# Kernel optimization log

Hardware: AMD Instinct MI355X
Metric: run time of the kernel (lower is better)

The kernel has to match this reference:

```python
import jax, jax.numpy as jnp
import numpy as np

B, S, A, D, m, M = 131072, 274, 30, 128, 6, 8
H1, Z = 256, 4
EPS_SINK, N_SINK = 0.05, 10
ETA0, ETA1 = 0.05, 0.15
ALPHA_MIN, ALPHA_MAX = 0.06, 0.3
W_R, W_S, W_C = 0.6, 0.25, 0.15
TECH_IDX = np.array([61, 91, 121, 151, 181, 211, 241, 271])


def setup_inputs() -> dict:
    key = jax.random.key(0)
    ks = jax.random.split(key, 24)
    rn = lambda k, shp, fan: (jax.random.normal(k, shp, jnp.float32) / np.sqrt(fan)).astype(jnp.float32)
    return {
        'state': jax.random.normal(ks[0], (B, S), jnp.float32),
        'fitness': jnp.ones((B, M), jnp.float32),
        # epitope_encoder: Linear(S,256) -> LayerNorm -> ReLU -> Linear(256, m*D)
        'we1': rn(ks[1], (S, H1), S), 'be1': jnp.zeros((H1,)),
        'ln_g': jnp.ones((H1,)), 'ln_b': jnp.zeros((H1,)),
        'we2': rn(ks[2], (H1, m * D), H1), 'be2': jnp.zeros((m * D,)),
        'proto_keys': rn(ks[3], (M, D), D),
        # M decoder MLPs: Linear(D,128)->ReLU->Linear(128,A)->Softplus (stacked)
        'wd1': rn(ks[4], (M, D, 128), D), 'bd1': jnp.zeros((M, 128)),
        'wd2': rn(ks[5], (M, 128, A), 128), 'bd2': jnp.zeros((M, A)),
        # TCellMinimal: Linear(12,D)->ReLU; heads for crisis types z and crisis_base
        'wt': rn(ks[6], (12, D), 12), 'bt': jnp.zeros((D,)),
        'wz': rn(ks[7], (D, Z), D), 'bz': jnp.zeros((Z,)),
        'wc': rn(ks[8], (D, 1), D), 'bc': jnp.zeros((1,)),
        'w_prev': jnp.full((1, M), 1.0 / M, jnp.float32),
        'crisis_bias': jnp.zeros((1,), jnp.float32),
    }


def _forward(state, fitness, we1, be1, ln_g, ln_b, we2, be2, proto_keys,
             wd1, bd1, wd2, bd2, wt, bt, wz, bz, wc, bc, w_prev, crisis_bias):
    # ---- market feature extraction ----
    balance = state[:, 0:1]
    prices = state[:, 1:31]
    shares = state[:, 31:61]
    price_mean = prices.mean(axis=1, keepdims=True)
    price_std = jnp.std(prices, axis=1, keepdims=True, ddof=1) + 1e-8  # torch .std is unbiased
    total_value = balance + (prices * shares).sum(axis=1, keepdims=True)
    cash_ratio = balance / (total_value + 1e-8)
    tech = state[:, TECH_IDX]
    mf = jnp.concatenate([balance, price_mean, price_std, cash_ratio, tech], axis=1)  # [B,12]
    # ---- TCellMinimal (reconstructed) ----
    h_t = jax.nn.relu(mf @ wt + bt)                # danger embedding [B,D]
    z = jax.nn.softmax(h_t @ wz + bz, axis=-1)     # crisis types [B,Z]
    crisis_base = jax.nn.sigmoid(h_t @ wc + bc)    # [B,1]
    danger = h_t
    # ---- crisis level ----
    delta_sharpe = state[:, -2:-1]
    cvar = state[:, -1:]
    ds_s = jax.nn.sigmoid(delta_sharpe * 10.0)
    cv_s = jax.nn.sigmoid(jnp.abs(cvar) * 50.0)
    crisis_level = W_R * crisis_base + W_S * ds_s + W_C * cv_s + crisis_bias  # [B,1]
    # ---- epitope encoder (eval mode: dropout off) ----
    h = state @ we1 + be1
    mu = h.mean(axis=-1, keepdims=True)
    var = ((h - mu) ** 2).mean(axis=-1, keepdims=True)
    h = (h - mu) * jax.lax.rsqrt(var + 1e-5) * ln_g + ln_b
    h = jax.nn.relu(h)
    E = (h @ we2 + be2).reshape(B, m, D)
    # ---- IRT (reconstructed): cosine cost + Sinkhorn OT + replicator mix ----
    En = E / (jnp.linalg.norm(E, axis=-1, keepdims=True) + 1e-8)
    Kn = proto_keys / (jnp.linalg.norm(proto_keys, axis=-1, keepdims=True) + 1e-8)
    dn = danger / (jnp.linalg.norm(danger, axis=-1, keepdims=True) + 1e-8)
    sim = jnp.einsum('bmd,jd->bmj', En, Kn)          # [B,m,M]
    dsim = jnp.einsum('bd,jd->bj', dn, Kn)           # [B,M]
    C = 1.0 - sim - 0.1 * dsim[:, None, :]           # cost matrix [B,m,M]
    logK = -C / EPS_SINK
    log_mu = -jnp.log(float(m))
    log_nu = -jnp.log(float(M))
    u = jnp.zeros((B, m), C.dtype)
    v = jnp.zeros((B, M), C.dtype)
    for _ in range(N_SINK):
        u = log_mu - jax.nn.logsumexp(logK + v[:, None, :], axis=2)
        v = log_nu - jax.nn.logsumexp(logK + u[:, :, None], axis=1)
    P = jnp.exp(logK + u[:, :, None] + v[:, None, :])  # transport plan [B,m,M]
    w_ot = P.sum(axis=1)
    w_ot = w_ot / (w_ot.sum(axis=-1, keepdims=True) + 1e-8)
    eta = ETA0 + ETA1 * crisis_level                   # [B,1]
    w_rep = w_prev * jnp.exp(eta * fitness)
    w_rep = w_rep / (w_rep.sum(axis=-1, keepdims=True) + 1e-8)
    alpha_c = jnp.clip(ALPHA_MAX - (ALPHA_MAX - ALPHA_MIN) * crisis_level, ALPHA_MIN, ALPHA_MAX)
    w = (1.0 - alpha_c) * w_rep + alpha_c * w_ot
    w = w / (w.sum(axis=-1, keepdims=True) + 1e-8)     # [B,M]
    # ---- per-prototype decoders (note: input K[:,j,:] is batch-constant) ----
    hd = jax.nn.relu(jnp.einsum('jd,jdh->jh', proto_keys, wd1) + bd1)
    conc = jax.nn.softplus(jnp.einsum('jh,jha->ja', hd, wd2) + bd2)  # [M,A]
    mixed_conc = jnp.einsum('bm,ma->ba', w, conc) + 1.0
    # deterministic=True path (Dirichlet mean proxy via softmax as in source)
    action = jax.nn.softmax(mixed_conc, axis=-1)
    action = jnp.clip(action, 0.0, 1.0)
    action = action / (action.sum(axis=-1, keepdims=True) + 1e-8)
    return action


def reference(state, fitness, we1, be1, ln_g, ln_b, we2, be2, proto_keys,
              wd1, bd1, wd2, bd2, wt, bt, wz, bz, wc, bc, w_prev, crisis_bias):
    return _forward(state, fitness, we1, be1, ln_g, ln_b, we2, be2, proto_keys,
                    wd1, bd1, wd2, bd2, wt, bt, wz, bz, wc, bc, w_prev, crisis_bias)
```

## Files before the change

### kernel.cpp

```cpp
#include <hip/hip_runtime.h>
#include <math.h>

#define B_TOT   131072
#define S_DIM   274
#define H1_DIM  256
#define M_EMB   6
#define M_POP   8
#define D_DIM   128
#define A_DIM   30

typedef __attribute__((ext_vector_type(8))) short bf16x8;
typedef __attribute__((ext_vector_type(4))) float f32x4;

__device__ __forceinline__ float sigmf(float x){ return 1.0f/(1.0f+__expf(-x)); }

__device__ __forceinline__ unsigned short f2bf(float f){
    union { float f; unsigned int u; } v; v.f = f;
    unsigned int r = v.u + 0x7FFFu + ((v.u >> 16) & 1u);
    return (unsigned short)(r >> 16);
}

__device__ __forceinline__ bf16x8 pack8(const float* v){
    bf16x8 r;
    #pragma unroll
    for (int j=0;j<8;++j) r[j] = (short)f2bf(v[j]);
    return r;
}

__global__ void k0a_precompute(const float* __restrict__ proto,
                               const float* __restrict__ wd1, const float* __restrict__ bd1,
                               const float* __restrict__ wd2, const float* __restrict__ bd2,
                               const float* __restrict__ we2, const float* __restrict__ be2,
                               float* __restrict__ Kn, float* __restrict__ conc,
                               float* __restrict__ W2K, float* __restrict__ bK)
{
    __shared__ float sKn[M_POP][D_DIM];
    __shared__ float sHd[M_POP][D_DIM];
    const int t = threadIdx.x;
    const int j = t >> 5, lane32 = t & 31;
    float ss = 0.f;
    for (int q = lane32; q < D_DIM; q += 32){ float v = proto[j*D_DIM+q]; ss += v*v; }
    #pragma unroll
    for (int mk = 16; mk >= 1; mk >>= 1) ss += __shfl_xor(ss, mk, 64);
    float inv = 1.0f / (sqrtf(ss) + 1e-8f);
    for (int q = lane32; q < D_DIM; q += 32){
        float kv = proto[j*D_DIM+q]*inv;
        Kn[j*D_DIM+q] = kv; sKn[j][q] = kv;
    }
    for (int h = lane32; h < D_DIM; h += 32){
        float acc = bd1[j*D_DIM+h];
        for (int d = 0; d < D_DIM; ++d)
            acc = fmaf(proto[j*D_DIM+d], wd1[(j*D_DIM+d)*D_DIM + h], acc);
        sHd[j][h] = fmaxf(acc, 0.f);
    }
    __syncthreads();
    if (t < M_POP*A_DIM){
        int jj = t / A_DIM, a = t - jj*A_DIM;
        float acc = bd2[jj*A_DIM + a];
        for (int h = 0; h < D_DIM; ++h)
            acc = fmaf(sHd[jj][h], wd2[(jj*D_DIM+h)*A_DIM + a], acc);
        float sp;
        if (acc > 20.f)       sp = acc;
        else if (acc < -20.f) sp = expf(acc);
        else                  sp = log1pf(expf(acc));
        conc[jj*A_DIM + a] = sp;
    }
    for (int o = t; o < 256*48; o += 256){
        int k = o / 48, pc = o - k*48;
        int jj = pc & 7, col0 = (pc >> 3) * 128;
        const float4* wrow = (const float4*)(we2 + (size_t)k*768 + col0);
        const float4* krow = (const float4*)(&sKn[jj][0]);
        float4 s4 = make_float4(0.f,0.f,0.f,0.f);
        #pragma unroll 8
        for (int dq = 0; dq < 32; ++dq){
            float4 wv = wrow[dq], kv = krow[dq];
            s4.x = fmaf(wv.x,kv.x,s4.x); s4.y = fmaf(wv.y,kv.y,s4.y);
            s4.z = fmaf(wv.z,kv.z,s4.z); s4.w = fmaf(wv.w,kv.w,s4.w);
        }
        W2K[o] = (s4.x+s4.y)+(s4.z+s4.w);
    }
    if (t < 48){
        int jj = t & 7, col0 = (t >> 3) * 128;
        const float4* brow = (const float4*)(be2 + col0);
        const float4* krow = (const float4*)(&sKn[jj][0]);
        float4 s4 = make_float4(0.f,0.f,0.f,0.f);
        #pragma unroll 8
        for (int dq = 0; dq < 32; ++dq){
            float4 bv = brow[dq], kv = krow[dq];
            s4.x = fmaf(bv.x,kv.x,s4.x); s4.y = fmaf(bv.y,kv.y,s4.y);
            s4.z = fmaf(bv.z,kv.z,s4.z); s4.w = fmaf(bv.w,kv.w,s4.w);
        }
        bK[t] = (s4.x+s4.y)+(s4.z+s4.w);
    }
}

__global__ void k0b_we1_frag(const float* __restrict__ we1, short* __restrict__ B1f)
{
    int s = blockIdx.x*256 + threadIdx.x;
    int ct = s / (9*64);
    int rem = s - ct*(9*64);
    int ks = rem >> 6, lam = rem & 63;
    int kb = 32*ks + (lam>>4)*8;
    int col = 16*ct + (lam&15);
    float v[8];
    #pragma unroll
    for (int j=0;j<8;++j){
        int k = kb + j;
        v[j] = (k < S_DIM) ? we1[(size_t)k*H1_DIM + col] : 0.f;
    }
    bf16x8 p = pack8(v);
    *(bf16x8*)(B1f + (size_t)s*8) = p;
}

__global__ void k0c_we2_frag(const float* __restrict__ we2, const float* __restrict__ W2K,
                             short* __restrict__ B2f)
{
    int s = blockIdx.x*256 + threadIdx.x;
    int ct = s / (8*64);
    int rem = s - ct*(8*64);
    int ks = rem >> 6, lam = rem & 63;
    int kb = 32*ks + (lam>>4)*8;
    int col = 16*ct + (lam&15);
    float v[8];
    #pragma unroll
    for (int j=0;j<8;++j){
        int k = kb + j;
        v[j] = (col < 768) ? we2[(size_t)k*768 + col] : W2K[k*48 + (col-768)];
    }
    bf16x8 p = pack8(v);
    *(bf16x8*)(B2f + (size_t)s*8) = p;
}

__global__ __launch_bounds__(256, 2)
void k1_h1_aux(const float* __restrict__ state, const short* __restrict__ B1f,
               const float* __restrict__ be1, const float* __restrict__ lng,
               const float* __restrict__ lnb, const float* __restrict__ wt,
               const float* __restrict__ bt,  const float* __restrict__ wc,
               const float* __restrict__ bc,  const float* __restrict__ crisis_bias,
               const float* __restrict__ Kn,
               short* __restrict__ h1b, float* __restrict__ crisL, float* __restrict__ dsimO)
{
    __shared__ short ldsB[2][8192];
    const int tid  = threadIdx.x;
    const int lane = tid & 63, w = tid >> 6;
    const int grp  = lane >> 4;
    const int row0 = blockIdx.x * 128;

    {
        const int r = tid >> 1, part = tid & 1;
        const float* srow = state + (size_t)(row0 + r) * S_DIM;
        float bal = srow[0];
        float sp = 0.f;
        for (int q = 1; q <= 30; ++q) sp += srow[q];
        float pmean = sp * (1.0f/30.0f);
        float sv = 0.f, tv = bal;
        for (int q = 1; q <= 30; ++q){
            float p = srow[q];
            float d = p - pmean; sv = fmaf(d,d,sv);
            tv = fmaf(p, srow[q+30], tv);
        }
        float pstd = sqrtf(sv * (1.0f/29.0f)) + 1e-8f;
        float cash = bal / (tv + 1e-8f);
        float mf[12];
        mf[0]=bal; mf[1]=pmean; mf[2]=pstd; mf[3]=cash;
        mf[4]=srow[61];  mf[5]=srow[91];   mf[6]=srow[121]; mf[7]=srow[151];
        mf[8]=srow[181]; mf[9]=srow[211];  mf[10]=srow[241]; mf[11]=srow[271];
        float csum=0.f, nsum=0.f;
        float ssum[M_POP];
        #pragma unroll
        for (int jj=0;jj<M_POP;++jj) ssum[jj]=0.f;
        const float4* wt4 = (const float4*)wt;
        const float4* bt4 = (const float4*)bt;
        const float4* wc4 = (const float4*)wc;
        const float4* Kn4 = (const float4*)Kn;
        for (int dq = 0; dq < 16; ++dq){
            int qi = part*16 + dq;
            float4 a = bt4[qi];
            #pragma unroll
            for (int f = 0; f < 12; ++f){
                float4 wv = wt4[f*32 + qi];
                a.x = fmaf(mf[f],wv.x,a.x); a.y = fmaf(mf[f],wv.y,a.y);
                a.z = fmaf(mf[f],wv.z,a.z); a.w = fmaf(mf[f],wv.w,a.w);
            }
            a.x=fmaxf(a.x,0.f); a.y=fmaxf(a.y,0.f); a.z=fmaxf(a.z,0.f); a.w=fmaxf(a.w,0.f);
            float4 cv = wc4[qi];
            csum += a.x*cv.x + a.y*cv.y + a.z*cv.z + a.w*cv.w;
            nsum += a.x*a.x + a.y*a.y + a.z*a.z + a.w*a.w;
            #pragma unroll
            for (int jj=0;jj<M_POP;++jj){
                float4 kv = Kn4[jj*32 + qi];
                ssum[jj] += a.x*kv.x + a.y*kv.y + a.z*kv.z + a.w*kv.w;
            }
        }
        csum += __shfl_xor(csum, 1, 64);
        nsum += __shfl_xor(nsum, 1, 64);
        #pragma unroll
        for (int jj=0;jj<M_POP;++jj) ssum[jj] += __shfl_xor(ssum[jj], 1, 64);
        if (part == 0){
            float cb  = sigmf(csum + bc[0]);
            float dss = sigmf(srow[272]*10.0f);
            float cvs = sigmf(fabsf(srow[273])*50.0f);
            crisL[row0+r] = 0.6f*cb + 0.25f*dss + 0.15f*cvs + crisis_bias[0];
            float invd = 1.0f/(sqrtf(nsum) + 1e-8f);
            #pragma unroll
            for (int jj=0;jj<M_POP;++jj) dsimO[(size_t)(row0+r)*M_POP + jj] = ssum[jj]*invd;
        }
    }

    bf16x8 Af[2][9];
    #pragma unroll
    for (int rt=0;rt<2;++rt){
        int row = row0 + w*32 + rt*16 + (lane&15);
        const float* sp = state + (size_t)row*S_DIM;
        #pragma unroll
        for (int ks=0;ks<9;++ks){
            float v[8];
            int kb = 32*ks + grp*8;
            if (ks < 8){
                #pragma unroll
                for (int h=0;h<4;++h){
                    float2 t2 = *(const float2*)(sp + kb + 2*h);
                    v[2*h] = t2.x; v[2*h+1] = t2.y;
                }
            } else {
                #pragma unroll
                for (int j2=0;j2<8;++j2) v[j2]=0.f;
                if (grp < 2){
                    #pragma unroll
                    for (int h=0;h<4;++h){
                        float2 t2 = *(const float2*)(sp + kb + 2*h);
                        v[2*h] = t2.x; v[2*h+1] = t2.y;
                    }
                } else if (grp == 2){
                    float2 t2 = *(const float2*)(sp + 272);
                    v[0] = t2.x; v[1] = t2.y;
                }
            }
            Af[rt][ks] = pack8(v);
        }
    }

    f32x4 acc[2][16];
    #pragma unroll
    for (int rt=0;rt<2;++rt)
        #pragma unroll
        for (int ct=0;ct<16;++ct) acc[rt][ct] = (f32x4){0.f,0.f,0.f,0.f};

    float4 vr[4];
    #pragma unroll
    for (int i=0;i<4;++i){
        int slot = i*256 + tid; int ctl = slot>>6, lam = slot&63;
        vr[i] = *(const float4*)(B1f + ((size_t)(ctl*9 + 0)*64 + lam)*8);
    }
    #pragma unroll
    for (int i=0;i<4;++i){
        int slot = i*256 + tid; int ctl = slot>>6, lam = slot&63;
        *(float4*)&ldsB[0][ctl*512 + lam*8] = vr[i];
    }
    __syncthreads();
    #pragma unroll
    for (int ks=0; ks<9; ++ks){
        if (ks < 8){
            #pragma unroll
            for (int i=0;i<4;++i){
                int slot = i*256 + tid; int ctl = slot>>6, lam = slot&63;
                vr[i] = *(const float4*)(B1f + ((size_t)(ctl*9 + ks+1)*64 + lam)*8);
            }
        }
        const int bo = (ks&1)*8192;
        #pragma unroll
        for (int ct=0; ct<16; ++ct){
            bf16x8 bf = *(const bf16x8*)&ldsB[0][bo + ct*512 + lane*8];
            acc[0][ct] = __builtin_amdgcn_mfma_f32_16x16x32_bf16(Af[0][ks], bf, acc[0][ct], 0,0,0);
            acc[1][ct] = __builtin_amdgcn_mfma_f32_16x16x32_bf16(Af[1][ks], bf, acc[1][ct], 0,0,0);
        }
        if (ks < 8){
            const int bo2 = ((ks+1)&1)*8192;
            #pragma unroll
            for (int i=0;i<4;++i){
                int slot = i*256 + tid; int ctl = slot>>6, lam = slot&63;
                *(float4*)&ldsB[0][bo2 + ctl*512 + lam*8] = vr[i];
            }
        }
        __syncthreads();
    }

    short* eLds = (short*)ldsB;
    const int wbase = w * 4096;
    #pragma unroll
    for (int rt=0;rt<2;++rt){
        float s[4] = {0.f,0.f,0.f,0.f};
        float sq[4] = {0.f,0.f,0.f,0.f};
        #pragma unroll
        for (int ct=0;ct<16;++ct){
            float be = be1[ct*16 + (lane&15)];
            #pragma unroll
            for (int r=0;r<4;++r){
                float h = acc[rt][ct][r] + be;
                acc[rt][ct][r] = h;
                s[r] += h; sq[r] = fmaf(h,h,sq[r]);
            }
        }
        #pragma unroll
        for (int mk=1; mk<=8; mk<<=1){
            #pragma unroll
            for (int r=0;r<4;++r){ s[r] += __shfl_xor(s[r],mk,64); sq[r] += __shfl_xor(sq[r],mk,64); }
        }
        float rstd[4], mu[4];
        #pragma unroll
        for (int r=0;r<4;++r){
            mu[r] = s[r] * (1.0f/256.0f);
            float var = sq[r]*(1.0f/256.0f) - mu[r]*mu[r];
            rstd[r] = rsqrtf(var + 1e-5f);
        }
        #pragma unroll
        for (int ct=0;ct<16;++ct){
            int col = ct*16 + (lane&15);
            float g = lng[col], bb = lnb[col];
            #pragma unroll
            for (int r=0;r<4;++r){
                float v = (acc[rt][ct][r]-mu[r])*rstd[r]*g + bb;
                v = fmaxf(v, 0.f);
                eLds[wbase + ((grp*4)+r)*256 + col] = (short)f2bf(v);
            }
        }
        int rowStart = row0 + w*32 + rt*16;
        #pragma unroll
        for (int i=0;i<8;++i){
            float4 d4 = *(const float4*)&eLds[wbase + (i*64 + lane)*8];
            *(float4*)(h1b + (size_t)rowStart*256 + (i*64+lane)*8) = d4;
        }
    }
}

template<int NCT>
__device__ __forceinline__ void k2_gemm_pass(f32x4 (&acc)[2][16], const bf16x8 (&Af)[2][8],
        short* ldsB, const short* __restrict__ B2f, int pass, int tid, int lane)
{
    #pragma unroll
    for (int rt=0;rt<2;++rt)
        #pragma unroll
        for (int ct=0;ct<NCT;++ct) acc[rt][ct] = (f32x4){0.f,0.f,0.f,0.f};
    float4 vr[4];
    #pragma unroll
    for (int i=0;i<4;++i){
        int slot = i*256 + tid;
        if (slot < NCT*64){ int ctl = slot>>6, lam = slot&63;
            vr[i] = *(const float4*)(B2f + ((size_t)((pass*16+ctl)*8 + 0)*64 + lam)*8); }
    }
    #pragma unroll
    for (int i=0;i<4;++i){
        int slot = i*256 + tid;
        if (slot < NCT*64){ int ctl = slot>>6, lam = slot&63;
            *(float4*)&ldsB[ctl*512 + lam*8] = vr[i]; }
    }
    __syncthreads();
    #pragma unroll
    for (int ks=0; ks<8; ++ks){
        if (ks < 7){
            #pragma unroll
            for (int i=0;i<4;++i){
                int slot = i*256 + tid;
                if (slot < NCT*64){ int ctl = slot>>6, lam = slot&63;
                    vr[i] = *(const float4*)(B2f + ((size_t)((pass*16+ctl)*8 + ks+1)*64 + lam)*8); }
            }
        }
        const int bo = (ks&1)*8192;
        #pragma unroll
        for (int ct=0; ct<NCT; ++ct){
            bf16x8 bf = *(const bf16x8*)&ldsB[bo + ct*512 + lane*8];
            acc[0][ct] = __builtin_amdgcn_mfma_f32_16x16x32_bf16(Af[0][ks], bf, acc[0][ct], 0,0,0);
            acc[1][ct] = __builtin_amdgcn_mfma_f32_16x16x32_bf16(Af[1][ks], bf, acc[1][ct], 0,0,0);
        }
        if (ks < 7){
            const int bo2 = ((ks+1)&1)*8192;
            #pragma unroll
            for (int i=0;i<4;++i){
                int slot = i*256 + tid;
                if (slot < NCT*64){ int ctl = slot>>6, lam = slot&63;
                    *(float4*)&ldsB[bo2 + ctl*512 + lam*8] = vr[i]; }
            }
        }
        __syncthreads();
    }
}

__global__ __launch_bounds__(256, 2)
void k2_emb_sink_out(const short* __restrict__ h1b, const short* __restrict__ B2f,
                     const float* __restrict__ be2, const float* __restrict__ bK,
                     const float* __restrict__ conc, const float* __restrict__ crisL,
                     const float* __restrict__ dsimI, const float* __restrict__ fitness,
                     const float* __restrict__ w_prev, float* __restrict__ out)
{
    __shared__ short ldsB[2][8192];
    __shared__ float sNrm[128*9];
    __shared__ float sSim[128*49];
    __shared__ float sConc[M_POP*A_DIM];
    const int tid  = threadIdx.x;
    const int lane = tid & 63, w = tid >> 6;
    const int grp  = lane >> 4;
    const int row0 = blockIdx.x * 128;

    for (int q = tid; q < M_POP*A_DIM; q += 256) sConc[q] = conc[q];

    bf16x8 Af[2][8];
    #pragma unroll
    for (int rt=0;rt<2;++rt){
        int row = row0 + w*32 + rt*16 + (lane&15);
        #pragma unroll
        for (int ks=0;ks<8;++ks)
            Af[rt][ks] = *(const bf16x8*)(h1b + (size_t)row*256 + 32*ks + grp*8);
    }

    f32x4 acc[2][16];
    #pragma unroll 1
    for (int pass=0; pass<3; ++pass){
        k2_gemm_pass<16>(acc, Af, &ldsB[0][0], B2f, pass, tid, lane);
        float nsq[2][4][2];
        #pragma unroll
        for (int rt=0;rt<2;++rt)
            #pragma unroll
            for (int r=0;r<4;++r){ nsq[rt][r][0]=0.f; nsq[rt][r][1]=0.f; }
        #pragma unroll
        for (int ct=0;ct<16;++ct){
            float be = be2[pass*256 + ct*16 + (lane&15)];
            const int hh = ct >> 3;
            #pragma unroll
            for (int rt=0;rt<2;++rt)
                #pragma unroll
                for (int r=0;r<4;++r){
                    float e = acc[rt][ct][r] + be;
                    nsq[rt][r][hh] = fmaf(e,e,nsq[rt][r][hh]);
                }
        }
        #pragma unroll
        for (int mk=1; mk<=8; mk<<=1){
            #pragma unroll
            for (int rt=0;rt<2;++rt)
                #pragma unroll
                for (int r=0;r<4;++r){
                    nsq[rt][r][0] += __shfl_xor(nsq[rt][r][0],mk,64);
                    nsq[rt][r][1] += __shfl_xor(nsq[rt][r][1],mk,64);
                }
        }
        if ((lane&15) < 2){
            int panel = 2*pass + (lane&15);
            #pragma unroll
            for (int rt=0;rt<2;++rt)
                #pragma unroll
                for (int r=0;r<4;++r){
                    int row = w*32 + rt*16 + grp*4 + r;
                    sNrm[row*9 + panel] = nsq[rt][r][lane&15];
                }
        }
        __syncthreads();
    }
    k2_gemm_pass<3>(acc, Af, &ldsB[0][0], B2f, 3, tid, lane);
    #pragma unroll
    for (int ct=0;ct<3;++ct){
        float bKv = bK[ct*16 + (lane&15)];
        #pragma unroll
        for (int rt=0;rt<2;++rt)
            #pragma unroll
            for (int r=0;r<4;++r){
                int row = w*32 + rt*16 + grp*4 + r;
                sSim[row*49 + ct*16 + (lane&15)] = acc[rt][ct][r] + bKv;
            }
    }
    __syncthreads();

    float* sAct = (float*)ldsB;
    if (tid < 128){
        const int grow = row0 + tid;
        float invn[M_EMB];
        #pragma unroll
        for (int i=0;i<M_EMB;++i) invn[i] = 1.0f/(sqrtf(sNrm[tid*9+i]) + 1e-8f);
        float logK[M_EMB][M_POP];
        #pragma unroll
        for (int i=0;i<M_EMB;++i){
            #pragma unroll
            for (int jj=0;jj<M_POP;++jj){
                float sim = sSim[tid*49 + i*8 + jj]*invn[i];
                float C = 1.0f - sim - 0.1f*dsimI[(size_t)grow*M_POP + jj];
                logK[i][jj] = -20.0f*C;
            }
        }
        const float LOG_MU = -1.7917594692280550f;
        const float LOG_NU = -2.0794415416798357f;
        float u[M_EMB], v[M_POP];
        #pragma unroll
        for (int i=0;i<M_EMB;++i) u[i]=0.f;
        #pragma unroll
        for (int jj=0;jj<M_POP;++jj) v[jj]=0.f;
        for (int it=0; it<10; ++it){
            #pragma unroll
            for (int i=0;i<M_EMB;++i){
                float mx = -1e30f;
                #pragma unroll
                for (int jj=0;jj<M_POP;++jj) mx = fmaxf(mx, logK[i][jj]+v[jj]);
                float sum = 0.f;
                #pragma unroll
                for (int jj=0;jj<M_POP;++jj) sum += __expf(logK[i][jj]+v[jj]-mx);
                u[i] = LOG_MU - (mx + __logf(sum));
            }
            #pragma unroll
            for (int jj=0;jj<M_POP;++jj){
                float mx = -1e30f;
                #pragma unroll
                for (int i=0;i<M_EMB;++i) mx = fmaxf(mx, logK[i][jj]+u[i]);
                float sum = 0.f;
                #pragma unroll
                for (int i=0;i<M_EMB;++i) sum += __expf(logK[i][jj]+u[i]-mx);
                v[jj] = LOG_NU - (mx + __logf(sum));
            }
        }
        float wot[M_POP]; float wsum = 0.f;
        #pragma unroll
        for (int jj=0;jj<M_POP;++jj){
            float sum = 0.f;
            #pragma unroll
            for (int i=0;i<M_EMB;++i) sum += __expf(logK[i][jj]+u[i]+v[jj]);
            wot[jj]=sum; wsum += sum;
        }
        float invw = 1.0f/(wsum + 1e-8f);
        float cl = crisL[grow];
        float eta = 0.05f + 0.15f*cl;
        float wrep[M_POP]; float rsum=0.f;
        #pragma unroll
        for (int jj=0;jj<M_POP;++jj){
            wrep[jj] = w_prev[jj]*__expf(eta*fitness[(size_t)grow*M_POP+jj]);
            rsum += wrep[jj];
        }
        float invr = 1.0f/(rsum + 1e-8f);
        float al = fminf(fmaxf(0.3f - 0.24f*cl, 0.06f), 0.3f);
        float wv[M_POP]; float ws2=0.f;
        #pragma unroll
        for (int jj=0;jj<M_POP;++jj){
            wv[jj] = (1.0f-al)*wrep[jj]*invr + al*wot[jj]*invw;
            ws2 += wv[jj];
        }
        float invw2 = 1.0f/(ws2 + 1e-8f);
        #pragma unroll
        for (int jj=0;jj<M_POP;++jj) wv[jj] *= invw2;
        float mc[A_DIM]; float mmax = -1e30f;
        #pragma unroll
        for (int a=0;a<A_DIM;++a){
            float sum = 1.0f;
            #pragma unroll
            for (int jj=0;jj<M_POP;++jj) sum = fmaf(wv[jj], sConc[jj*A_DIM+a], sum);
            mc[a]=sum; mmax = fmaxf(mmax, sum);
        }
        float es = 0.f;
        #pragma unroll
        for (int a=0;a<A_DIM;++a){ mc[a] = __expf(mc[a]-mmax); es += mc[a]; }
        float inve = 1.0f/es;
        float s3 = 0.f;
        #pragma unroll
        for (int a=0;a<A_DIM;++a){ mc[a] *= inve; s3 += mc[a]; }
        float invf = 1.0f/(s3 + 1e-8f);
        #pragma unroll
        for (int a=0;a<A_DIM;++a) sAct[tid*A_DIM + a] = mc[a]*invf;
    }
    __syncthreads();
    for (int q = tid; q < 128*A_DIM; q += 256)
        out[(size_t)row0*A_DIM + q] = sAct[q];
}

extern "C" void kernel_launch(void* const* d_in, const int* in_sizes, int n_in,
                              void* d_out, int out_size, void* d_ws, size_t ws_size,
                              hipStream_t stream)
{
    const float* state       = (const float*)d_in[0];
    const float* fitness     = (const float*)d_in[1];
    const float* we1         = (const float*)d_in[2];
    const float* be1         = (const float*)d_in[3];
    const float* lng         = (const float*)d_in[4];
    const float* lnb         = (const float*)d_in[5];
    const float* we2         = (const float*)d_in[6];
    const float* be2         = (const float*)d_in[7];
    const float* proto       = (const float*)d_in[8];
    const float* wd1         = (const float*)d_in[9];
    const float* bd1         = (const float*)d_in[10];
    const float* wd2         = (const float*)d_in[11];
    const float* bd2         = (const float*)d_in[12];
    const float* wt          = (const float*)d_in[13];
    const float* bt          = (const float*)d_in[14];
    const float* wc          = (const float*)d_in[17];
    const float* bc          = (const float*)d_in[18];
    const float* w_prev      = (const float*)d_in[19];
    const float* crisis_bias = (const float*)d_in[20];

    float* ws = (float*)d_ws;
    short* h1b   = (short*)ws;
    float* crisL = ws + (size_t)B_TOT*128;
    float* dsim  = crisL + B_TOT;
    float* Kn    = dsim + (size_t)B_TOT*8;
    float* conc  = Kn + 1024;
    float* W2K   = conc + 256;
    float* bK    = W2K + 12288;
    short* B1f   = (short*)(bK + 64);
    short* B2f   = (short*)(bK + 64 + 36864);
    float* outp  = (float*)d_out;

    k0a_precompute<<<1, 256, 0, stream>>>(proto, wd1, bd1, wd2, bd2, we2, be2,
                                          Kn, conc, W2K, bK);
    k0b_we1_frag<<<36, 256, 0, stream>>>(we1, B1f);
    k0c_we2_frag<<<102, 256, 0, stream>>>(we2, W2K, B2f);
    k1_h1_aux<<<B_TOT/128, 256, 0, stream>>>(state, B1f, be1, lng, lnb,
                                             wt, bt, wc, bc, crisis_bias, Kn,
                                             h1b, crisL, dsim);
    k2_emb_sink_out<<<B_TOT/128, 256, 0, stream>>>(h1b, B2f, be2, bK, conc,
                                                   crisL, dsim, fitness, w_prev, outp);
}
```

Before: 779.0 us.

## Load GEMM B fragments directly from global and split precompute kernel

Removes the LDS double-buffered staging of the pre-fragmented weight matrices in both main GEMM kernels. Each wave now reads its bf16 B fragments straight from global memory (L2-resident), eight at a time, which drops the per-k-step __syncthreads and LDS traffic. The single-block precompute kernel is also split into three kernels so the decoder and W2K work spread over several blocks. The cost is redundant global or L2 reads of the weights by every wave, plus two more kernel launches.

```diff
diff --git a/kernel.cpp b/kernel.cpp
--- a/kernel.cpp
+++ b/kernel.cpp
@@ -27,15 +27,8 @@
     return r;
 }
 
-__global__ void k0a_precompute(const float* __restrict__ proto,
-                               const float* __restrict__ wd1, const float* __restrict__ bd1,
-                               const float* __restrict__ wd2, const float* __restrict__ bd2,
-                               const float* __restrict__ we2, const float* __restrict__ be2,
-                               float* __restrict__ Kn, float* __restrict__ conc,
-                               float* __restrict__ W2K, float* __restrict__ bK)
-{
-    __shared__ float sKn[M_POP][D_DIM];
-    __shared__ float sHd[M_POP][D_DIM];
+__global__ void k0a_kn(const float* __restrict__ proto, float* __restrict__ Kn)
+{
     const int t = threadIdx.x;
     const int j = t >> 5, lane32 = t & 31;
     float ss = 0.f;
@@ -43,33 +36,47 @@
     #pragma unroll
     for (int mk = 16; mk >= 1; mk >>= 1) ss += __shfl_xor(ss, mk, 64);
     float inv = 1.0f / (sqrtf(ss) + 1e-8f);
-    for (int q = lane32; q < D_DIM; q += 32){
-        float kv = proto[j*D_DIM+q]*inv;
-        Kn[j*D_DIM+q] = kv; sKn[j][q] = kv;
-    }
-    for (int h = lane32; h < D_DIM; h += 32){
-        float acc = bd1[j*D_DIM+h];
+    for (int q = lane32; q < D_DIM; q += 32) Kn[j*D_DIM+q] = proto[j*D_DIM+q]*inv;
+}
+
+__global__ void k0h_conc(const float* __restrict__ proto,
+                         const float* __restrict__ wd1, const float* __restrict__ bd1,
+                         const float* __restrict__ wd2, const float* __restrict__ bd2,
+                         float* __restrict__ conc)
+{
+    __shared__ float sHd[D_DIM];
+    const int j = blockIdx.x;
+    const int t = threadIdx.x;
+    if (t < D_DIM){
+        float acc = bd1[j*D_DIM + t];
         for (int d = 0; d < D_DIM; ++d)
-            acc = fmaf(proto[j*D_DIM+d], wd1[(j*D_DIM+d)*D_DIM + h], acc);
-        sHd[j][h] = fmaxf(acc, 0.f);
+            acc = fmaf(proto[j*D_DIM+d], wd1[(j*D_DIM+d)*D_DIM + t], acc);
+        sHd[t] = fmaxf(acc, 0.f);
     }
     __syncthreads();
-    if (t < M_POP*A_DIM){
-        int jj = t / A_DIM, a = t - jj*A_DIM;
-        float acc = bd2[jj*A_DIM + a];
+    if (t < A_DIM){
+        float acc = bd2[j*A_DIM + t];
         for (int h = 0; h < D_DIM; ++h)
-            acc = fmaf(sHd[jj][h], wd2[(jj*D_DIM+h)*A_DIM + a], acc);
+            acc = fmaf(sHd[h], wd2[(j*D_DIM+h)*A_DIM + t], acc);
         float sp;
         if (acc > 20.f)       sp = acc;
         else if (acc < -20.f) sp = expf(acc);
         else                  sp = log1pf(expf(acc));
-        conc[jj*A_DIM + a] = sp;
-    }
-    for (int o = t; o < 256*48; o += 256){
+        conc[j*A_DIM + t] = sp;
+    }
+}
+
+__global__ void k0w_w2k(const float* __restrict__ we2, const float* __restrict__ be2,
+                        const float* __restrict__ Kn,
+                        float* __restrict__ W2K, float* __restrict__ bK)
+{
+    const int t = threadIdx.x;
+    if (blockIdx.x < 48){
+        int o = blockIdx.x*256 + t;
         int k = o / 48, pc = o - k*48;
         int jj = pc & 7, col0 = (pc >> 3) * 128;
         const float4* wrow = (const float4*)(we2 + (size_t)k*768 + col0);
-        const float4* krow = (const float4*)(&sKn[jj][0]);
+        const float4* krow = (const float4*)(Kn + jj*D_DIM);
         float4 s4 = make_float4(0.f,0.f,0.f,0.f);
         #pragma unroll 8
         for (int dq = 0; dq < 32; ++dq){
@@ -78,11 +85,10 @@
             s4.z = fmaf(wv.z,kv.z,s4.z); s4.w = fmaf(wv.w,kv.w,s4.w);
         }
         W2K[o] = (s4.x+s4.y)+(s4.z+s4.w);
-    }
-    if (t < 48){
+    } else if (t < 48){
         int jj = t & 7, col0 = (t >> 3) * 128;
         const float4* brow = (const float4*)(be2 + col0);
-        const float4* krow = (const float4*)(&sKn[jj][0]);
+        const float4* krow = (const float4*)(Kn + jj*D_DIM);
         float4 s4 = make_float4(0.f,0.f,0.f,0.f);
         #pragma unroll 8
         for (int dq = 0; dq < 32; ++dq){
@@ -140,7 +146,7 @@
                const float* __restrict__ Kn,
                short* __restrict__ h1b, float* __restrict__ crisL, float* __restrict__ dsimO)
 {
-    __shared__ short ldsB[2][8192];
+    __shared__ short eLds[4][4096];
     const int tid  = threadIdx.x;
     const int lane = tid & 63, w = tid >> 6;
     const int grp  = lane >> 4;
@@ -246,47 +252,27 @@
         #pragma unroll
         for (int ct=0;ct<16;++ct) acc[rt][ct] = (f32x4){0.f,0.f,0.f,0.f};
 
-    float4 vr[4];
-    #pragma unroll
-    for (int i=0;i<4;++i){
-        int slot = i*256 + tid; int ctl = slot>>6, lam = slot&63;
-        vr[i] = *(const float4*)(B1f + ((size_t)(ctl*9 + 0)*64 + lam)*8);
-    }
-    #pragma unroll
-    for (int i=0;i<4;++i){
-        int slot = i*256 + tid; int ctl = slot>>6, lam = slot&63;
-        *(float4*)&ldsB[0][ctl*512 + lam*8] = vr[i];
-    }
-    __syncthreads();
+    const short* bb = B1f + (size_t)lane*8;
     #pragma unroll
     for (int ks=0; ks<9; ++ks){
-        if (ks < 8){
-            #pragma unroll
-            for (int i=0;i<4;++i){
-                int slot = i*256 + tid; int ctl = slot>>6, lam = slot&63;
-                vr[i] = *(const float4*)(B1f + ((size_t)(ctl*9 + ks+1)*64 + lam)*8);
-            }
-        }
-        const int bo = (ks&1)*8192;
-        #pragma unroll
-        for (int ct=0; ct<16; ++ct){
-            bf16x8 bf = *(const bf16x8*)&ldsB[0][bo + ct*512 + lane*8];
-            acc[0][ct] = __builtin_amdgcn_mfma_f32_16x16x32_bf16(Af[0][ks], bf, acc[0][ct], 0,0,0);
-            acc[1][ct] = __builtin_amdgcn_mfma_f32_16x16x32_bf16(Af[1][ks], bf, acc[1][ct], 0,0,0);
-        }
-        if (ks < 8){
-            const int bo2 = ((ks+1)&1)*8192;
-            #pragma unroll
-            for (int i=0;i<4;++i){
-                int slot = i*256 + tid; int ctl = slot>>6, lam = slot&63;
-                *(float4*)&ldsB[0][bo2 + ctl*512 + lam*8] = vr[i];
-            }
-        }
-        __syncthreads();
-    }
-
-    short* eLds = (short*)ldsB;
-    const int wbase = w * 4096;
+        #pragma unroll
+        for (int g=0; g<2; ++g){
+            bf16x8 bf[8];
+            #pragma unroll
+            for (int q=0;q<8;++q){
+                int ct = g*8+q;
+                bf[q] = *(const bf16x8*)(bb + (size_t)ct*4608 + ks*512);
+            }
+            #pragma unroll
+            for (int q=0;q<8;++q){
+                int ct = g*8+q;
+                acc[0][ct] = __builtin_amdgcn_mfma_f32_16x16x32_bf16(Af[0][ks], bf[q], acc[0][ct], 0,0,0);
+                acc[1][ct] = __builtin_amdgcn_mfma_f32_16x16x32_bf16(Af[1][ks], bf[q], acc[1][ct], 0,0,0);
+            }
+        }
+    }
+
+    const int wbase = w;
     #pragma unroll
     for (int rt=0;rt<2;++rt){
         float s[4] = {0.f,0.f,0.f,0.f};
@@ -316,18 +302,18 @@
         #pragma unroll
         for (int ct=0;ct<16;++ct){
             int col = ct*16 + (lane&15);
-            float g = lng[col], bb = lnb[col];
+            float g = lng[col], bb2 = lnb[col];
             #pragma unroll
             for (int r=0;r<4;++r){
-                float v = (acc[rt][ct][r]-mu[r])*rstd[r]*g + bb;
+                float v = (acc[rt][ct][r]-mu[r])*rstd[r]*g + bb2;
                 v = fmaxf(v, 0.f);
-                eLds[wbase + ((grp*4)+r)*256 + col] = (short)f2bf(v);
+                eLds[wbase][((grp*4)+r)*256 + col] = (short)f2bf(v);
             }
         }
         int rowStart = row0 + w*32 + rt*16;
         #pragma unroll
         for (int i=0;i<8;++i){
-            float4 d4 = *(const float4*)&eLds[wbase + (i*64 + lane)*8];
+            float4 d4 = *(const float4*)&eLds[wbase][(i*64 + lane)*8];
             *(float4*)(h1b + (size_t)rowStart*256 + (i*64+lane)*8) = d4;
         }
     }
@@ -335,53 +321,32 @@
 
 template<int NCT>
 __device__ __forceinline__ void k2_gemm_pass(f32x4 (&acc)[2][16], const bf16x8 (&Af)[2][8],
-        short* ldsB, const short* __restrict__ B2f, int pass, int tid, int lane)
+        const short* __restrict__ pb)
 {
     #pragma unroll
     for (int rt=0;rt<2;++rt)
         #pragma unroll
         for (int ct=0;ct<NCT;++ct) acc[rt][ct] = (f32x4){0.f,0.f,0.f,0.f};
-    float4 vr[4];
-    #pragma unroll
-    for (int i=0;i<4;++i){
-        int slot = i*256 + tid;
-        if (slot < NCT*64){ int ctl = slot>>6, lam = slot&63;
-            vr[i] = *(const float4*)(B2f + ((size_t)((pass*16+ctl)*8 + 0)*64 + lam)*8); }
-    }
-    #pragma unroll
-    for (int i=0;i<4;++i){
-        int slot = i*256 + tid;
-        if (slot < NCT*64){ int ctl = slot>>6, lam = slot&63;
-            *(float4*)&ldsB[ctl*512 + lam*8] = vr[i]; }
-    }
-    __syncthreads();
     #pragma unroll
     for (int ks=0; ks<8; ++ks){
-        if (ks < 7){
-            #pragma unroll
-            for (int i=0;i<4;++i){
-                int slot = i*256 + tid;
-                if (slot < NCT*64){ int ctl = slot>>6, lam = slot&63;
-                    vr[i] = *(const float4*)(B2f + ((size_t)((pass*16+ctl)*8 + ks+1)*64 + lam)*8); }
-            }
-        }
-        const int bo = (ks&1)*8192;
-        #pragma unroll
-        for (int ct=0; ct<NCT; ++ct){
-            bf16x8 bf = *(const bf16x8*)&ldsB[bo + ct*512 + lane*8];
-            acc[0][ct] = __builtin_amdgcn_mfma_f32_16x16x32_bf16(Af[0][ks], bf, acc[0][ct], 0,0,0);
-            acc[1][ct] = __builtin_amdgcn_mfma_f32_16x16x32_bf16(Af[1][ks], bf, acc[1][ct], 0,0,0);
-        }
-        if (ks < 7){
-            const int bo2 = ((ks+1)&1)*8192;
-            #pragma unroll
-            for (int i=0;i<4;++i){
-                int slot = i*256 + tid;
-                if (slot < NCT*64){ int ctl = slot>>6, lam = slot&63;
-                    *(float4*)&ldsB[bo2 + ctl*512 + lam*8] = vr[i]; }
-            }
-        }
-        __syncthreads();
+        #pragma unroll
+        for (int g=0; g<(NCT+7)/8; ++g){
+            bf16x8 bf[8];
+            #pragma unroll
+            for (int q=0;q<8;++q){
+                int ct = g*8+q;
+                if (ct < NCT)
+                    bf[q] = *(const bf16x8*)(pb + (size_t)ct*4096 + ks*512);
+            }
+            #pragma unroll
+            for (int q=0;q<8;++q){
+                int ct = g*8+q;
+                if (ct < NCT){
+                    acc[0][ct] = __builtin_amdgcn_mfma_f32_16x16x32_bf16(Af[0][ks], bf[q], acc[0][ct], 0,0,0);
+                    acc[1][ct] = __builtin_amdgcn_mfma_f32_16x16x32_bf16(Af[1][ks], bf[q], acc[1][ct], 0,0,0);
+                }
+            }
+        }
     }
 }
 
@@ -392,10 +357,10 @@
                      const float* __restrict__ dsimI, const float* __restrict__ fitness,
                      const float* __restrict__ w_prev, float* __restrict__ out)
 {
-    __shared__ short ldsB[2][8192];
     __shared__ float sNrm[128*9];
     __shared__ float sSim[128*49];
     __shared__ float sConc[M_POP*A_DIM];
+    __shared__ float sAct[128*A_DIM];
     const int tid  = threadIdx.x;
     const int lane = tid & 63, w = tid >> 6;
     const int grp  = lane >> 4;
@@ -412,10 +377,11 @@
             Af[rt][ks] = *(const bf16x8*)(h1b + (size_t)row*256 + 32*ks + grp*8);
     }
 
+    const short* bbase = B2f + (size_t)lane*8;
     f32x4 acc[2][16];
     #pragma unroll 1
     for (int pass=0; pass<3; ++pass){
-        k2_gemm_pass<16>(acc, Af, &ldsB[0][0], B2f, pass, tid, lane);
+        k2_gemm_pass<16>(acc, Af, bbase + (size_t)pass*65536);
         float nsq[2][4][2];
         #pragma unroll
         for (int rt=0;rt<2;++rt)
@@ -453,9 +419,8 @@
                     sNrm[row*9 + panel] = nsq[rt][r][lane&15];
                 }
         }
-        __syncthreads();
-    }
-    k2_gemm_pass<3>(acc, Af, &ldsB[0][0], B2f, 3, tid, lane);
+    }
+    k2_gemm_pass<3>(acc, Af, bbase + (size_t)3*65536);
     #pragma unroll
     for (int ct=0;ct<3;++ct){
         float bKv = bK[ct*16 + (lane&15)];
@@ -469,7 +434,6 @@
     }
     __syncthreads();
 
-    float* sAct = (float*)ldsB;
     if (tid < 128){
         const int grow = row0 + tid;
         float invn[M_EMB];
@@ -602,8 +566,9 @@
     short* B2f   = (short*)(bK + 64 + 36864);
     float* outp  = (float*)d_out;
 
-    k0a_precompute<<<1, 256, 0, stream>>>(proto, wd1, bd1, wd2, bd2, we2, be2,
-                                          Kn, conc, W2K, bK);
+    k0a_kn<<<1, 256, 0, stream>>>(proto, Kn);
+    k0h_conc<<<8, 128, 0, stream>>>(proto, wd1, bd1, wd2, bd2, conc);
+    k0w_w2k<<<49, 256, 0, stream>>>(we2, be2, Kn, W2K, bK);
     k0b_we1_frag<<<36, 256, 0, stream>>>(we1, B1f);
     k0c_we2_frag<<<102, 256, 0, stream>>>(we2, W2K, B2f);
     k1_h1_aux<<<B_TOT/128, 256, 0, stream>>>(state, B1f, be1, lng, lnb,
```

After: 743.3 us. 4.6% less time.
